# Kernel tuning notes

Hardware: AMD Instinct MI355X
Metric: run time of the kernel (lower is better)

## Reference

```python
import jax, jax.numpy as jnp
import numpy as np

B, H, W = 32, 64, 64
D = 8        # input_dim (capsule dim of incoming caps)
C = 8        # input_ch (number of incoming capsule types)
DIM = 8      # dim_capsule (output capsule dim)
NCH = 8      # n_channels (number of output capsule types)


def _gconv(x, w, groups, stride=1):
    # x: NHWC, w: HWIO with I = in_ch/groups, O = total out (grouped by output blocks)
    return jax.lax.conv_general_dilated(
        x, w, (stride, stride), 'SAME',
        dimension_numbers=('NHWC', 'HWIO', 'NHWC'),
        feature_group_count=groups)


def setup_inputs():
    key = jax.random.key(0)
    ks = jax.random.split(key, 5)
    inputs = jax.random.normal(ks[0], (B, H, W, D, C), jnp.float32)
    Att_W = jax.random.normal(ks[1], (1, 1, DIM, C, C * NCH), jnp.float32) * 0.05
    ConvTrans_W = jax.random.normal(ks[2], (3, 3, D, C * DIM * NCH), jnp.float32) * 0.05
    ConvTrans_B = jnp.zeros((C * DIM * NCH,), jnp.float32)
    FeaExt_W = jax.random.normal(ks[3], (3, 3, DIM, DIM * NCH), jnp.float32) * 0.05
    FeaExt_B = jnp.zeros((DIM * NCH,), jnp.float32)
    CapsAct_W = jax.random.normal(ks[4], (1, 1, DIM, DIM * NCH), jnp.float32) * 0.05
    CapsAct_B = jnp.zeros((DIM * NCH,), jnp.float32)
    return {'inputs': inputs, 'Att_W': Att_W, 'ConvTrans_W': ConvTrans_W,
            'ConvTrans_B': ConvTrans_B, 'FeaExt_W': FeaExt_W, 'FeaExt_B': FeaExt_B,
            'CapsAct_W': CapsAct_W, 'CapsAct_B': CapsAct_B}


def reference(inputs, Att_W, ConvTrans_W, ConvTrans_B, FeaExt_W, FeaExt_B,
              CapsAct_W, CapsAct_B):
    # --- ConvTrans: per input-capsule-type 3x3 conv (== grouped conv over C groups) ---
    # inputs [B,H,W,D,C] -> [B,H,W,C*D] with group-major ordering
    xt = jnp.transpose(inputs, (0, 1, 2, 4, 3)).reshape(B, H, W, C * D)
    # ConvTrans_W [3,3,D, C*DIM*NCH]: output block i is the kernel for input group i
    y = _gconv(xt, ConvTrans_W, groups=C) + ConvTrans_B  # [B,H,W, C*DIM*NCH]
    # -> u[b,h,w,d,c_in,n]  (matches concat+transpose in the original)
    u = y.reshape(B, H, W, C, DIM, NCH).transpose(0, 1, 2, 4, 3, 5)

    # --- Attention: conv3d with kernel [1,1,DIM,C,C] per output type n (VALID over DIM) ---
    # Att_W [1,1,DIM,C,C*NCH] -> A[d, c_in, n, c_out]
    A = Att_W[0, 0].reshape(DIM, C, NCH, C)
    att = jnp.einsum('bhwdcn,dcno->bhwon', u, A)       # [B,H,W,C,NCH]
    att = jax.nn.softmax(att, axis=3)                  # softmax over input_ch
    v = jnp.einsum('bhwdon,bhwon->bhwdn', u, att)      # weighted sum over input_ch

    # --- FeaExt (3x3, grouped over NCH) + ReLU, then CapsAct (1x1, grouped) ---
    vt = jnp.transpose(v, (0, 1, 2, 4, 3)).reshape(B, H, W, NCH * DIM)
    h1 = jax.nn.relu(_gconv(vt, FeaExt_W, groups=NCH) + FeaExt_B)
    h2 = _gconv(h1, CapsAct_W, groups=NCH) + CapsAct_B
    out = h2.reshape(B, H, W, NCH, DIM).transpose(0, 1, 2, 4, 3)  # [B,H,W,DIM,NCH]
    return out
```

## Files before the change

kernel.cpp:

```cpp
#include <hip/hip_runtime.h>

#define HH 64
#define WW 64

typedef _Float16 f16;
typedef f16 f16x8 __attribute__((ext_vector_type(8)));
typedef f16 f16x4 __attribute__((ext_vector_type(4)));
typedef f16 f16x2 __attribute__((ext_vector_type(2)));
typedef float f32x4 __attribute__((ext_vector_type(4)));

#define M1_H 0
#define BU_H 49152
#define BF_H 98304
#define BC_H 110592
#define VT_H 114688
#define PREP_N (64 + 114688)

union U2 { f16x2 v; int i; };

__global__ __launch_bounds__(256) void prep_kernel(
    const float* __restrict__ attw, const float* __restrict__ ctw,
    const float* __restrict__ ctb, const float* __restrict__ few,
    const float* __restrict__ caw, float* __restrict__ ws) {
  int i = blockIdx.x * 256 + threadIdx.x;
  if (i >= PREP_N) return;
  f16* hb = (f16*)(ws + 64);
  if (i < 64) {
    int s = i >> 4, l15 = i & 15;
    int o = 2 * s + (l15 >> 3), n = l15 & 7;
    float acc = 0.f;
    for (int c = 0; c < 8; ++c)
      for (int d = 0; d < 8; ++d)
        acc += ctb[c * 64 + d * 8 + n] * attw[d * 512 + c * 64 + n * 8 + o];
    ws[i] = acc;
    return;
  }
  int z = i - 64;
  if (z < BU_H) {
    int j = z & 7, lane = (z >> 3) & 63, rest = z >> 9;
    int rs = rest % 12, c = rest / 12;
    int r = rs >> 2, s = rs & 3;
    int q = lane >> 4, l15 = lane & 15;
    int t = r * 4 + q;
    int o = 2 * s + (l15 >> 3), n = l15 & 7;
    float acc = 0.f;
    if (t < 9)
      for (int d = 0; d < 8; ++d)
        acc += ctw[(t * 8 + j) * 512 + c * 64 + d * 8 + n] *
               attw[d * 512 + c * 64 + n * 8 + o];
    hb[M1_H + z] = (f16)acc;
  } else if (z < BF_H) {
    int z2 = z - BU_H;
    int j = z2 & 7, lane = (z2 >> 3) & 63, rest = z2 >> 9;
    int rs = rest % 12, c = rest / 12;
    int r = rs >> 2, s = rs & 3;
    int q = lane >> 4, l15 = lane & 15;
    int t = r * 4 + q;
    int d = 2 * s + (l15 >> 3), n = l15 & 7;
    float v = (t < 9) ? ctw[(t * 8 + j) * 512 + c * 64 + d * 8 + n] : 0.f;
    hb[z] = (f16)v;
  } else if (z < BC_H) {
    int z2 = z - BF_H;
    int j = z2 & 7, lane = (z2 >> 3) & 63, rest = z2 >> 9;
    int r = rest % 3, g = rest / 3;
    int q = lane >> 4, l15 = lane & 15;
    int t = r * 4 + q;
    int d = 2 * (j & 3) + (j >> 2);
    float v = 0.f;
    if (t < 9 && ((l15 >> 3) == (g & 1)))
      v = few[(t * 8 + d) * 64 + g * 8 + (l15 & 7)];
    hb[z] = (f16)v;
  } else if (z < VT_H) {
    int z2 = z - BC_H;
    int j = z2 & 7, lane = (z2 >> 3) & 63, rest = z2 >> 9;
    int s = rest & 3, c2 = rest >> 2;
    int q = lane >> 4, l15 = lane & 15;
    int nk = c2 * 4 + q;
    int nc = 2 * s + (l15 >> 3);
    float v = (nk == nc) ? caw[j * 64 + nc * 8 + (l15 & 7)] : 0.f;
    hb[z] = (f16)v;
  }
}

__global__ __launch_bounds__(256, 2) void caps_stage1(
    const float* __restrict__ in, const float* __restrict__ ws,
    const float* __restrict__ ctb, f16* __restrict__ vt) {
  __shared__ f16 xt[181 * 72];
  int bid = blockIdx.x;
  int b = bid >> 5, t5 = bid & 31;
  int ty = t5 >> 3, tx = t5 & 7;
  int tid = threadIdx.x;

  for (int i = tid; i < 181 * 8; i += 256) {
    int c = i & 7, hp = i >> 3;
    float xs[8] = {0.f, 0.f, 0.f, 0.f, 0.f, 0.f, 0.f, 0.f};
    if (hp < 180) {
      int hy = hp / 10, hx = hp - hy * 10;
      int gy = ty * 16 + hy - 1, gx = tx * 8 + hx - 1;
      if (gy >= 0 && gy < HH && gx >= 0 && gx < WW) {
        const float* src = in + (((b * HH + gy) * WW + gx) * 64 + c);
#pragma unroll
        for (int d = 0; d < 8; ++d) xs[d] = src[d * 8];
      }
    }
    f16x8 pk;
#pragma unroll
    for (int d = 0; d < 8; ++d) pk[d] = (f16)xs[d];
    *(f16x8*)&xt[hp * 72 + c * 8] = pk;
  }
  __syncthreads();

  int w = __builtin_amdgcn_readfirstlane(tid >> 6);
  int lane = tid & 63;
  int q = lane >> 4, l15 = lane & 15;
  int h = l15 >> 3, n = l15 & 7;

  int hpt[2][3];
#pragma unroll
  for (int i2 = 0; i2 < 2; ++i2) {
    int pyA = (2 * w + i2) * 2 + h;
    int pxA = l15 & 7;
#pragma unroll
    for (int r = 0; r < 3; ++r) {
      int t = r * 4 + q;
      int hp = 180;
      if (t < 9) {
        int ky = t / 3, kx = t - ky * 3;
        hp = (pyA + ky) * 10 + pxA + kx;
      }
      hpt[i2][r] = hp * 72;
    }
  }

  const f16x8* m1v = (const f16x8*)((const f16*)(ws + 64) + M1_H);
  const f16x8* buv = (const f16x8*)((const f16*)(ws + 64) + BU_H);
  const float* lb = ws;

  f32x4 L[2][4];
#pragma unroll
  for (int s = 0; s < 4; ++s) {
    float v0 = lb[s * 16 + l15];
    L[0][s] = (f32x4){v0, v0, v0, v0};
    L[1][s] = (f32x4){v0, v0, v0, v0};
  }
#pragma unroll 1
  for (int c = 0; c < 8; ++c) {
    f16x8 bm[12];
#pragma unroll
    for (int rs = 0; rs < 12; ++rs) bm[rs] = m1v[(c * 12 + rs) * 64 + lane];
    f16x8 a[2][3];
#pragma unroll
    for (int i2 = 0; i2 < 2; ++i2)
#pragma unroll
      for (int r = 0; r < 3; ++r)
        a[i2][r] = *(const f16x8*)&xt[hpt[i2][r] + c * 8];
#pragma unroll
    for (int i2 = 0; i2 < 2; ++i2)
#pragma unroll
      for (int s = 0; s < 4; ++s)
#pragma unroll
        for (int r = 0; r < 3; ++r)
          L[i2][s] = __builtin_amdgcn_mfma_f32_16x16x32_f16(
              a[i2][r], bm[r * 4 + s], L[i2][s], 0, 0, 0);
  }

  f16x8 P8[2][4];
#pragma unroll
  for (int i2 = 0; i2 < 2; ++i2)
#pragma unroll
    for (int r = 0; r < 4; ++r) {
      float v0 = L[i2][0][r], v1 = L[i2][1][r], v2 = L[i2][2][r], v3 = L[i2][3][r];
      float pm = fmaxf(fmaxf(v0, v1), fmaxf(v2, v3));
      float m = fmaxf(pm, __shfl_xor(pm, 8));
      float e0 = __expf(v0 - m), e1 = __expf(v1 - m);
      float e2 = __expf(v2 - m), e3 = __expf(v3 - m);
      float ps = e0 + e1 + e2 + e3;
      float inv = 1.f / (ps + __shfl_xor(ps, 8));
      f16 o0 = (f16)(e0 * inv), o1 = (f16)(e1 * inv);
      f16 o2 = (f16)(e2 * inv), o3 = (f16)(e3 * inv);
      U2 p01, p23, r01, r23;
      p01.v = (f16x2){o0, o1};
      p23.v = (f16x2){o2, o3};
      r01.i = __shfl_xor(p01.i, 8);
      r23.i = __shfl_xor(p23.i, 8);
      f16x8 t;
      t[0] = h ? r01.v[0] : o0;
      t[1] = h ? o0 : r01.v[0];
      t[2] = h ? r01.v[1] : o1;
      t[3] = h ? o1 : r01.v[1];
      t[4] = h ? r23.v[0] : o2;
      t[5] = h ? o2 : r23.v[0];
      t[6] = h ? r23.v[1] : o3;
      t[7] = h ? o3 : r23.v[1];
      P8[i2][r] = t;
    }

  f32x4 V[2][4];
#pragma unroll
  for (int s = 0; s < 4; ++s) {
    V[0][s] = (f32x4){0.f, 0.f, 0.f, 0.f};
    V[1][s] = (f32x4){0.f, 0.f, 0.f, 0.f};
  }
#pragma unroll 1
  for (int c = 0; c < 8; ++c) {
    f16x8 bu[12];
#pragma unroll
    for (int rs = 0; rs < 12; ++rs) bu[rs] = buv[(c * 12 + rs) * 64 + lane];
    f16x8 a[2][3];
#pragma unroll
    for (int i2 = 0; i2 < 2; ++i2)
#pragma unroll
      for (int r = 0; r < 3; ++r)
        a[i2][r] = *(const f16x8*)&xt[hpt[i2][r] + c * 8];
    f32x4 U[2][4];
#pragma unroll
    for (int s = 0; s < 4; ++s) {
      float bv = ctb[c * 64 + s * 16 + l15];
      U[0][s] = (f32x4){bv, bv, bv, bv};
      U[1][s] = (f32x4){bv, bv, bv, bv};
    }
#pragma unroll
    for (int i2 = 0; i2 < 2; ++i2)
#pragma unroll
      for (int s = 0; s < 4; ++s)
#pragma unroll
        for (int r = 0; r < 3; ++r)
          U[i2][s] = __builtin_amdgcn_mfma_f32_16x16x32_f16(
              a[i2][r], bu[r * 4 + s], U[i2][s], 0, 0, 0);
#pragma unroll
    for (int i2 = 0; i2 < 2; ++i2)
#pragma unroll
      for (int r = 0; r < 4; ++r) {
        float af = (float)P8[i2][r][c];
#pragma unroll
        for (int s = 0; s < 4; ++s) V[i2][s][r] += U[i2][s][r] * af;
      }
  }

  __syncthreads();
  f16* vtmp = xt;
#pragma unroll
  for (int i2 = 0; i2 < 2; ++i2)
#pragma unroll
    for (int r = 0; r < 4; ++r) {
      int p = (2 * w + i2) * 16 + q * 4 + r;
      f16x4 st;
#pragma unroll
      for (int s = 0; s < 4; ++s) st[s] = (f16)V[i2][s][r];
      *(f16x4*)&vtmp[p * 72 + n * 8 + h * 4] = st;
    }
  __syncthreads();
  for (int idx = tid; idx < 1024; idx += 256) {
    int p = idx >> 3, q2 = idx & 7;
    float4 val = *(float4*)&vtmp[p * 72 + q2 * 8];
    int gy = ty * 16 + (p >> 3), gx = tx * 8 + (p & 7);
    ((float4*)(vt + ((b * HH + gy) * WW + gx) * 64))[q2] = val;
  }
}

__global__ __launch_bounds__(256, 2) void caps_stage2(
    const f16* __restrict__ vt, const float* __restrict__ ws,
    const float* __restrict__ fb, const float* __restrict__ cab,
    float* __restrict__ out) {
  __shared__ f16 smem[181 * 72];
  f16* vtile = smem;
  int bid = blockIdx.x;
  int b = bid >> 5, t5 = bid & 31;
  int ty = t5 >> 3, tx = t5 & 7;
  int tid = threadIdx.x;

  for (int i = tid; i < 181 * 8; i += 256) {
    int q2 = i & 7, hp = i >> 3;
    float4 val = make_float4(0.f, 0.f, 0.f, 0.f);
    if (hp < 180) {
      int hy = hp / 10, hx = hp - hy * 10;
      int gy = ty * 16 + hy - 1, gx = tx * 8 + hx - 1;
      if (gy >= 0 && gy < HH && gx >= 0 && gx < WW)
        val = ((const float4*)(vt + ((b * HH + gy) * WW + gx) * 64))[q2];
    }
    *(float4*)&vtile[hp * 72 + q2 * 8] = val;
  }
  __syncthreads();

  int w = __builtin_amdgcn_readfirstlane(tid >> 6);
  int lane = tid & 63;
  int q = lane >> 4, l15 = lane & 15;
  int h = l15 >> 3, j7 = l15 & 7;

  int hpt[2][3];
#pragma unroll
  for (int i2 = 0; i2 < 2; ++i2) {
    int pyA = (2 * w + i2) * 2 + h;
#pragma unroll
    for (int r = 0; r < 3; ++r) {
      int t = r * 4 + q;
      int hp = 180;
      if (t < 9) {
        int ky = t / 3, kx = t - ky * 3;
        hp = (pyA + ky) * 10 + j7 + kx;
      }
      hpt[i2][r] = hp * 72;
    }
  }

  const f16x8* bfv = (const f16x8*)((const f16*)(ws + 64) + BF_H);
  const f16x8* bcv = (const f16x8*)((const f16*)(ws + 64) + BC_H);

  f32x4 L[2][4];
#pragma unroll
  for (int s = 0; s < 4; ++s) {
    float bvv = fb[(2 * s + h) * 8 + j7];
    L[0][s] = (f32x4){bvv, bvv, bvv, bvv};
    L[1][s] = (f32x4){bvv, bvv, bvv, bvv};
  }
#pragma unroll
  for (int g = 0; g < 8; ++g) {
    int sg = g >> 1;
#pragma unroll
    for (int r = 0; r < 3; ++r) {
      f16x8 bf = bfv[(g * 3 + r) * 64 + lane];
#pragma unroll
      for (int i2 = 0; i2 < 2; ++i2) {
        f16x8 a = *(const f16x8*)&vtile[hpt[i2][r] + g * 8];
        L[i2][sg] = __builtin_amdgcn_mfma_f32_16x16x32_f16(a, bf, L[i2][sg], 0, 0, 0);
      }
    }
  }
#pragma unroll
  for (int i2 = 0; i2 < 2; ++i2)
#pragma unroll
    for (int s = 0; s < 4; ++s)
#pragma unroll
      for (int r = 0; r < 4; ++r) L[i2][s][r] = fmaxf(L[i2][s][r], 0.f);

  __syncthreads();
  f16* h1t = smem;
#pragma unroll
  for (int i2 = 0; i2 < 2; ++i2)
#pragma unroll
    for (int s = 0; s < 4; ++s)
#pragma unroll
      for (int r = 0; r < 4; ++r)
        h1t[((2 * w + i2) * 16 + q * 4 + r) * 72 + (2 * s + h) * 8 + j7] =
            (f16)L[i2][s][r];
  __syncthreads();

  f32x4 H[2][4];
#pragma unroll
  for (int s = 0; s < 4; ++s) {
    float bvv = cab[(2 * s + h) * 8 + j7];
    H[0][s] = (f32x4){bvv, bvv, bvv, bvv};
    H[1][s] = (f32x4){bvv, bvv, bvv, bvv};
  }
#pragma unroll
  for (int c2 = 0; c2 < 2; ++c2) {
    f16x8 a2[2];
#pragma unroll
    for (int i2 = 0; i2 < 2; ++i2)
      a2[i2] = *(const f16x8*)&h1t[((2 * w + i2) * 16 + l15) * 72 + c2 * 32 + q * 8];
#pragma unroll
    for (int s = 0; s < 4; ++s) {
      f16x8 bc = bcv[(c2 * 4 + s) * 64 + lane];
#pragma unroll
      for (int i2 = 0; i2 < 2; ++i2)
        H[i2][s] = __builtin_amdgcn_mfma_f32_16x16x32_f16(a2[i2], bc, H[i2][s], 0, 0, 0);
    }
  }

  __syncthreads();
  float* outbuf = (float*)smem;
#pragma unroll
  for (int hh = 0; hh < 2; ++hh) {
    if ((w >> 1) == hh) {
#pragma unroll
      for (int i2 = 0; i2 < 2; ++i2)
#pragma unroll
        for (int s = 0; s < 4; ++s)
#pragma unroll
          for (int r = 0; r < 4; ++r) {
            int p = ((2 * w + i2) * 16 + q * 4 + r) - hh * 64;
            outbuf[p * 68 + j7 * 8 + 2 * s + h] = H[i2][s][r];
          }
    }
    __syncthreads();
    for (int idx = tid; idx < 1024; idx += 256) {
      int p = idx >> 4, q4 = idx & 15;
      float4 val = *(float4*)&outbuf[p * 68 + q4 * 4];
      int gp = hh * 64 + p;
      int gy = ty * 16 + (gp >> 3), gx = tx * 8 + (gp & 7);
      *(float4*)(out + ((b * HH + gy) * WW + gx) * 64 + q4 * 4) = val;
    }
    if (hh == 0) __syncthreads();
  }
}

extern "C" void kernel_launch(void* const* d_in, const int* in_sizes, int n_in,
                              void* d_out, int out_size, void* d_ws, size_t ws_size,
                              hipStream_t stream) {
  const float* inputs = (const float*)d_in[0];
  const float* attw   = (const float*)d_in[1];
  const float* ctw    = (const float*)d_in[2];
  const float* ctb    = (const float*)d_in[3];
  const float* few    = (const float*)d_in[4];
  const float* fb     = (const float*)d_in[5];
  const float* caw    = (const float*)d_in[6];
  const float* cab    = (const float*)d_in[7];
  float* out = (float*)d_out;
  float* ws  = (float*)d_ws;
  f16* vt = (f16*)(ws + 64) + VT_H;

  prep_kernel<<<(PREP_N + 255) / 256, 256, 0, stream>>>(attw, ctw, ctb, few, caw, ws);
  caps_stage1<<<32 * 32, 256, 0, stream>>>(inputs, ws, ctb, vt);
  caps_stage2<<<32 * 32, 256, 0, stream>>>(vt, ws, fb, cab, out);
}
```

Measured before the change: 151.3 us.

## Fuse both capsule stages into one kernel with halo recompute of attention output

Merges stage1 (ConvTrans, attention, softmax, weighted sum) and stage2 (FeaExt plus CapsAct) into a single kernel. Each block loads a 2-pixel input halo and recomputes v over the 10x18 halo region, so the intermediate fp16 v tensor no longer goes through global memory and one launch is dropped. The cost is about 40% more stage-1 MFMA work for the halo pixels, more shared memory and registers (3 row groups per wave), and lower occupancy risk. B-operand loads are also restructured per s to cut register pressure.

```diff
diff --git a/kernel.cpp b/kernel.cpp
--- a/kernel.cpp
+++ b/kernel.cpp
@@ -13,7 +13,6 @@
 #define BU_H 49152
 #define BF_H 98304
 #define BC_H 110592
-#define VT_H 114688
 #define PREP_N (64 + 114688)
 
 union U2 { f16x2 v; int i; };
@@ -70,7 +69,7 @@
     if (t < 9 && ((l15 >> 3) == (g & 1)))
       v = few[(t * 8 + d) * 64 + g * 8 + (l15 & 7)];
     hb[z] = (f16)v;
-  } else if (z < VT_H) {
+  } else {
     int z2 = z - BC_H;
     int j = z2 & 7, lane = (z2 >> 3) & 63, rest = z2 >> 9;
     int s = rest & 3, c2 = rest >> 2;
@@ -82,21 +81,23 @@
   }
 }
 
-__global__ __launch_bounds__(256, 2) void caps_stage1(
+__global__ __launch_bounds__(256, 2) void caps_fused(
     const float* __restrict__ in, const float* __restrict__ ws,
-    const float* __restrict__ ctb, f16* __restrict__ vt) {
-  __shared__ f16 xt[181 * 72];
+    const float* __restrict__ ctb, const float* __restrict__ fb,
+    const float* __restrict__ cab, float* __restrict__ out) {
+  __shared__ f16 smem[241 * 72];
   int bid = blockIdx.x;
   int b = bid >> 5, t5 = bid & 31;
   int ty = t5 >> 3, tx = t5 & 7;
   int tid = threadIdx.x;
 
-  for (int i = tid; i < 181 * 8; i += 256) {
-    int c = i & 7, hp = i >> 3;
+  f16* xt = smem;
+  for (int i = tid; i < 241 * 8; i += 256) {
+    int c = i & 7, xp = i >> 3;
     float xs[8] = {0.f, 0.f, 0.f, 0.f, 0.f, 0.f, 0.f, 0.f};
-    if (hp < 180) {
-      int hy = hp / 10, hx = hp - hy * 10;
-      int gy = ty * 16 + hy - 1, gx = tx * 8 + hx - 1;
+    if (xp < 240) {
+      int xy = xp / 12, xx = xp - xy * 12;
+      int gy = ty * 16 + xy - 2, gx = tx * 8 + xx - 2;
       if (gy >= 0 && gy < HH && gx >= 0 && gx < WW) {
         const float* src = in + (((b * HH + gy) * WW + gx) * 64 + c);
 #pragma unroll
@@ -106,7 +107,7 @@
     f16x8 pk;
 #pragma unroll
     for (int d = 0; d < 8; ++d) pk[d] = (f16)xs[d];
-    *(f16x8*)&xt[hp * 72 + c * 8] = pk;
+    *(f16x8*)&xt[xp * 72 + c * 8] = pk;
   }
   __syncthreads();
 
@@ -115,20 +116,20 @@
   int q = lane >> 4, l15 = lane & 15;
   int h = l15 >> 3, n = l15 & 7;
 
-  int hpt[2][3];
-#pragma unroll
-  for (int i2 = 0; i2 < 2; ++i2) {
-    int pyA = (2 * w + i2) * 2 + h;
-    int pxA = l15 & 7;
+  int hpt[3][3];
+#pragma unroll
+  for (int i3 = 0; i3 < 3; ++i3) {
+    int vp = (3 * w + i3) * 16 + l15;
+    int ry = vp / 10, rx = vp - ry * 10;
 #pragma unroll
     for (int r = 0; r < 3; ++r) {
       int t = r * 4 + q;
-      int hp = 180;
-      if (t < 9) {
+      int hp = 240;
+      if (t < 9 && vp < 180) {
         int ky = t / 3, kx = t - ky * 3;
-        hp = (pyA + ky) * 10 + pxA + kx;
-      }
-      hpt[i2][r] = hp * 72;
+        hp = (ry + ky) * 12 + rx + kx;
+      }
+      hpt[i3][r] = hp * 72;
     }
   }
 
@@ -136,40 +137,42 @@
   const f16x8* buv = (const f16x8*)((const f16*)(ws + 64) + BU_H);
   const float* lb = ws;
 
-  f32x4 L[2][4];
+  f32x4 L[3][4];
 #pragma unroll
   for (int s = 0; s < 4; ++s) {
     float v0 = lb[s * 16 + l15];
     L[0][s] = (f32x4){v0, v0, v0, v0};
     L[1][s] = (f32x4){v0, v0, v0, v0};
+    L[2][s] = (f32x4){v0, v0, v0, v0};
   }
 #pragma unroll 1
   for (int c = 0; c < 8; ++c) {
-    f16x8 bm[12];
-#pragma unroll
-    for (int rs = 0; rs < 12; ++rs) bm[rs] = m1v[(c * 12 + rs) * 64 + lane];
-    f16x8 a[2][3];
-#pragma unroll
-    for (int i2 = 0; i2 < 2; ++i2)
+    f16x8 a[3][3];
+#pragma unroll
+    for (int i3 = 0; i3 < 3; ++i3)
 #pragma unroll
       for (int r = 0; r < 3; ++r)
-        a[i2][r] = *(const f16x8*)&xt[hpt[i2][r] + c * 8];
-#pragma unroll
-    for (int i2 = 0; i2 < 2; ++i2)
-#pragma unroll
-      for (int s = 0; s < 4; ++s)
+        a[i3][r] = *(const f16x8*)&xt[hpt[i3][r] + c * 8];
+#pragma unroll
+    for (int s = 0; s < 4; ++s) {
+      f16x8 bm[3];
+#pragma unroll
+      for (int r = 0; r < 3; ++r) bm[r] = m1v[(c * 12 + r * 4 + s) * 64 + lane];
+#pragma unroll
+      for (int i3 = 0; i3 < 3; ++i3)
 #pragma unroll
         for (int r = 0; r < 3; ++r)
-          L[i2][s] = __builtin_amdgcn_mfma_f32_16x16x32_f16(
-              a[i2][r], bm[r * 4 + s], L[i2][s], 0, 0, 0);
-  }
-
-  f16x8 P8[2][4];
-#pragma unroll
-  for (int i2 = 0; i2 < 2; ++i2)
+          L[i3][s] = __builtin_amdgcn_mfma_f32_16x16x32_f16(
+              a[i3][r], bm[r], L[i3][s], 0, 0, 0);
+    }
+  }
+
+  f16x8 P8[3][4];
+#pragma unroll
+  for (int i3 = 0; i3 < 3; ++i3)
 #pragma unroll
     for (int r = 0; r < 4; ++r) {
-      float v0 = L[i2][0][r], v1 = L[i2][1][r], v2 = L[i2][2][r], v3 = L[i2][3][r];
+      float v0 = L[i3][0][r], v1 = L[i3][1][r], v2 = L[i3][2][r], v3 = L[i3][3][r];
       float pm = fmaxf(fmaxf(v0, v1), fmaxf(v2, v3));
       float m = fmaxf(pm, __shfl_xor(pm, 8));
       float e0 = __expf(v0 - m), e1 = __expf(v1 - m);
@@ -192,126 +195,90 @@
       t[5] = h ? o2 : r23.v[0];
       t[6] = h ? r23.v[1] : o3;
       t[7] = h ? o3 : r23.v[1];
-      P8[i2][r] = t;
-    }
-
-  f32x4 V[2][4];
+      P8[i3][r] = t;
+    }
+
+  f32x4 V[3][4];
 #pragma unroll
   for (int s = 0; s < 4; ++s) {
     V[0][s] = (f32x4){0.f, 0.f, 0.f, 0.f};
     V[1][s] = (f32x4){0.f, 0.f, 0.f, 0.f};
+    V[2][s] = (f32x4){0.f, 0.f, 0.f, 0.f};
   }
 #pragma unroll 1
   for (int c = 0; c < 8; ++c) {
-    f16x8 bu[12];
-#pragma unroll
-    for (int rs = 0; rs < 12; ++rs) bu[rs] = buv[(c * 12 + rs) * 64 + lane];
-    f16x8 a[2][3];
-#pragma unroll
-    for (int i2 = 0; i2 < 2; ++i2)
+    f16x8 a[3][3];
+#pragma unroll
+    for (int i3 = 0; i3 < 3; ++i3)
 #pragma unroll
       for (int r = 0; r < 3; ++r)
-        a[i2][r] = *(const f16x8*)&xt[hpt[i2][r] + c * 8];
-    f32x4 U[2][4];
+        a[i3][r] = *(const f16x8*)&xt[hpt[i3][r] + c * 8];
+    float af[3][4];
+#pragma unroll
+    for (int i3 = 0; i3 < 3; ++i3)
+#pragma unroll
+      for (int r = 0; r < 4; ++r) af[i3][r] = (float)P8[i3][r][c];
 #pragma unroll
     for (int s = 0; s < 4; ++s) {
+      f16x8 bu[3];
+#pragma unroll
+      for (int r = 0; r < 3; ++r) bu[r] = buv[(c * 12 + r * 4 + s) * 64 + lane];
       float bv = ctb[c * 64 + s * 16 + l15];
-      U[0][s] = (f32x4){bv, bv, bv, bv};
-      U[1][s] = (f32x4){bv, bv, bv, bv};
-    }
-#pragma unroll
-    for (int i2 = 0; i2 < 2; ++i2)
-#pragma unroll
-      for (int s = 0; s < 4; ++s)
+#pragma unroll
+      for (int i3 = 0; i3 < 3; ++i3) {
+        f32x4 U = (f32x4){bv, bv, bv, bv};
 #pragma unroll
         for (int r = 0; r < 3; ++r)
-          U[i2][s] = __builtin_amdgcn_mfma_f32_16x16x32_f16(
-              a[i2][r], bu[r * 4 + s], U[i2][s], 0, 0, 0);
-#pragma unroll
-    for (int i2 = 0; i2 < 2; ++i2)
-#pragma unroll
-      for (int r = 0; r < 4; ++r) {
-        float af = (float)P8[i2][r][c];
-#pragma unroll
-        for (int s = 0; s < 4; ++s) V[i2][s][r] += U[i2][s][r] * af;
-      }
-  }
-
-  __syncthreads();
-  f16* vtmp = xt;
-#pragma unroll
-  for (int i2 = 0; i2 < 2; ++i2)
+          U = __builtin_amdgcn_mfma_f32_16x16x32_f16(a[i3][r], bu[r], U, 0, 0, 0);
+#pragma unroll
+        for (int r = 0; r < 4; ++r) V[i3][s][r] += U[r] * af[i3][r];
+      }
+    }
+  }
+
+  __syncthreads();
+  f16* vtile = smem;
+#pragma unroll
+  for (int i3 = 0; i3 < 3; ++i3)
 #pragma unroll
     for (int r = 0; r < 4; ++r) {
-      int p = (2 * w + i2) * 16 + q * 4 + r;
+      int vrow = (3 * w + i3) * 16 + q * 4 + r;
+      int ry = vrow / 10, rx = vrow - ry * 10;
+      int gyv = ty * 16 + ry - 1, gxv = tx * 8 + rx - 1;
+      bool ok = (vrow < 180) && (gyv >= 0) && (gyv < HH) &&
+                (gxv >= 0) && (gxv < WW);
       f16x4 st;
 #pragma unroll
-      for (int s = 0; s < 4; ++s) st[s] = (f16)V[i2][s][r];
-      *(f16x4*)&vtmp[p * 72 + n * 8 + h * 4] = st;
-    }
-  __syncthreads();
-  for (int idx = tid; idx < 1024; idx += 256) {
-    int p = idx >> 3, q2 = idx & 7;
-    float4 val = *(float4*)&vtmp[p * 72 + q2 * 8];
-    int gy = ty * 16 + (p >> 3), gx = tx * 8 + (p & 7);
-    ((float4*)(vt + ((b * HH + gy) * WW + gx) * 64))[q2] = val;
-  }
-}
-
-__global__ __launch_bounds__(256, 2) void caps_stage2(
-    const f16* __restrict__ vt, const float* __restrict__ ws,
-    const float* __restrict__ fb, const float* __restrict__ cab,
-    float* __restrict__ out) {
-  __shared__ f16 smem[181 * 72];
-  f16* vtile = smem;
-  int bid = blockIdx.x;
-  int b = bid >> 5, t5 = bid & 31;
-  int ty = t5 >> 3, tx = t5 & 7;
-  int tid = threadIdx.x;
-
-  for (int i = tid; i < 181 * 8; i += 256) {
-    int q2 = i & 7, hp = i >> 3;
-    float4 val = make_float4(0.f, 0.f, 0.f, 0.f);
-    if (hp < 180) {
-      int hy = hp / 10, hx = hp - hy * 10;
-      int gy = ty * 16 + hy - 1, gx = tx * 8 + hx - 1;
-      if (gy >= 0 && gy < HH && gx >= 0 && gx < WW)
-        val = ((const float4*)(vt + ((b * HH + gy) * WW + gx) * 64))[q2];
-    }
-    *(float4*)&vtile[hp * 72 + q2 * 8] = val;
-  }
-  __syncthreads();
-
-  int w = __builtin_amdgcn_readfirstlane(tid >> 6);
-  int lane = tid & 63;
-  int q = lane >> 4, l15 = lane & 15;
-  int h = l15 >> 3, j7 = l15 & 7;
-
-  int hpt[2][3];
+      for (int s = 0; s < 4; ++s) st[s] = ok ? (f16)V[i3][s][r] : (f16)0.f;
+      *(f16x4*)&vtile[vrow * 72 + n * 8 + h * 4] = st;
+    }
+  __syncthreads();
+
+  int hpt2[2][3];
 #pragma unroll
   for (int i2 = 0; i2 < 2; ++i2) {
     int pyA = (2 * w + i2) * 2 + h;
 #pragma unroll
     for (int r = 0; r < 3; ++r) {
       int t = r * 4 + q;
-      int hp = 180;
+      int hp = 240;
       if (t < 9) {
         int ky = t / 3, kx = t - ky * 3;
-        hp = (pyA + ky) * 10 + j7 + kx;
-      }
-      hpt[i2][r] = hp * 72;
+        hp = (pyA + ky) * 10 + n + kx;
+      }
+      hpt2[i2][r] = hp * 72;
     }
   }
 
   const f16x8* bfv = (const f16x8*)((const f16*)(ws + 64) + BF_H);
   const f16x8* bcv = (const f16x8*)((const f16*)(ws + 64) + BC_H);
 
-  f32x4 L[2][4];
+  f32x4 G[2][4];
 #pragma unroll
   for (int s = 0; s < 4; ++s) {
-    float bvv = fb[(2 * s + h) * 8 + j7];
-    L[0][s] = (f32x4){bvv, bvv, bvv, bvv};
-    L[1][s] = (f32x4){bvv, bvv, bvv, bvv};
+    float bvv = fb[(2 * s + h) * 8 + n];
+    G[0][s] = (f32x4){bvv, bvv, bvv, bvv};
+    G[1][s] = (f32x4){bvv, bvv, bvv, bvv};
   }
 #pragma unroll
   for (int g = 0; g < 8; ++g) {
@@ -321,8 +288,8 @@
       f16x8 bf = bfv[(g * 3 + r) * 64 + lane];
 #pragma unroll
       for (int i2 = 0; i2 < 2; ++i2) {
-        f16x8 a = *(const f16x8*)&vtile[hpt[i2][r] + g * 8];
-        L[i2][sg] = __builtin_amdgcn_mfma_f32_16x16x32_f16(a, bf, L[i2][sg], 0, 0, 0);
+        f16x8 a = *(const f16x8*)&vtile[hpt2[i2][r] + g * 8];
+        G[i2][sg] = __builtin_amdgcn_mfma_f32_16x16x32_f16(a, bf, G[i2][sg], 0, 0, 0);
       }
     }
   }
@@ -331,7 +298,7 @@
 #pragma unroll
     for (int s = 0; s < 4; ++s)
 #pragma unroll
-      for (int r = 0; r < 4; ++r) L[i2][s][r] = fmaxf(L[i2][s][r], 0.f);
+      for (int r = 0; r < 4; ++r) G[i2][s][r] = fmaxf(G[i2][s][r], 0.f);
 
   __syncthreads();
   f16* h1t = smem;
@@ -341,14 +308,14 @@
     for (int s = 0; s < 4; ++s)
 #pragma unroll
       for (int r = 0; r < 4; ++r)
-        h1t[((2 * w + i2) * 16 + q * 4 + r) * 72 + (2 * s + h) * 8 + j7] =
-            (f16)L[i2][s][r];
+        h1t[((2 * w + i2) * 16 + q * 4 + r) * 72 + (2 * s + h) * 8 + n] =
+            (f16)G[i2][s][r];
   __syncthreads();
 
   f32x4 H[2][4];
 #pragma unroll
   for (int s = 0; s < 4; ++s) {
-    float bvv = cab[(2 * s + h) * 8 + j7];
+    float bvv = cab[(2 * s + h) * 8 + n];
     H[0][s] = (f32x4){bvv, bvv, bvv, bvv};
     H[1][s] = (f32x4){bvv, bvv, bvv, bvv};
   }
@@ -379,7 +346,7 @@
 #pragma unroll
           for (int r = 0; r < 4; ++r) {
             int p = ((2 * w + i2) * 16 + q * 4 + r) - hh * 64;
-            outbuf[p * 68 + j7 * 8 + 2 * s + h] = H[i2][s][r];
+            outbuf[p * 68 + n * 8 + 2 * s + h] = H[i2][s][r];
           }
     }
     __syncthreads();
@@ -407,9 +374,7 @@
   const float* cab    = (const float*)d_in[7];
   float* out = (float*)d_out;
   float* ws  = (float*)d_ws;
-  f16* vt = (f16*)(ws + 64) + VT_H;
 
   prep_kernel<<<(PREP_N + 255) / 256, 256, 0, stream>>>(attw, ctw, ctb, few, caw, ws);
-  caps_stage1<<<32 * 32, 256, 0, stream>>>(inputs, ws, ctb, vt);
-  caps_stage2<<<32 * 32, 256, 0, stream>>>(vt, ws, fb, cab, out);
+  caps_fused<<<32 * 32, 256, 0, stream>>>(inputs, ws, ctb, fb, cab, out);
 }
```

New measurement: 173.8 us. 1.15x slower.
